# Performance work log

Measured on AMD Instinct MI355X. Metric: run time of the kernel, lower is better.

## Reference

```python
import jax, jax.numpy as jnp
import numpy as np

N_EMBD = 1024
N_HEAD = 16
B, T = 4, 2048

def setup_inputs() -> dict:
    key = jax.random.key(0)
    ks = jax.random.split(key, 5)
    C = N_EMBD
    s = 0.02
    return {
        "x": jax.random.normal(ks[0], (B, T, C), dtype=jnp.float32),
        "W_attn": jax.random.normal(ks[1], (C, 3 * C), dtype=jnp.float32) * s,
        "b_attn": jnp.zeros((3 * C,), dtype=jnp.float32),
        "W_proj": jax.random.normal(ks[2], (C, C), dtype=jnp.float32) * s,
        "b_proj": jnp.zeros((C,), dtype=jnp.float32),
    }

def reference(x, W_attn, b_attn, W_proj, b_proj):
    Bz, Tz, C = x.shape
    H = N_HEAD
    hd = C // H
    qkv = x @ W_attn + b_attn                      # [B,T,3C]
    q, k, v = jnp.split(qkv, 3, axis=-1)
    # [B,H,T,hd]
    q = q.reshape(Bz, Tz, H, hd).transpose(0, 2, 1, 3)
    k = k.reshape(Bz, Tz, H, hd).transpose(0, 2, 1, 3)
    v = v.reshape(Bz, Tz, H, hd).transpose(0, 2, 1, 3)
    att = jnp.einsum('bhqd,bhkd->bhqk', q, k) * (1.0 / np.sqrt(hd))
    causal = jnp.tril(jnp.ones((Tz, Tz), dtype=bool))
    att = jnp.where(causal, att, -jnp.inf)
    att = jax.nn.softmax(att, axis=-1)
    y = jnp.einsum('bhqk,bhkd->bhqd', att, v)      # [B,H,T,hd]
    y = y.transpose(0, 2, 1, 3).reshape(Bz, Tz, C)
    return y @ W_proj + b_proj
```

## Files before the change

### kernel.cpp

```cpp
#include <hip/hip_runtime.h>
#include <hip/hip_bf16.h>

#define NEMBD 1024
#define NHEAD 16
#define HD    64
#define BB    4
#define TT    2048
#define MM    (BB*TT)
#define NQKV  (3*NEMBD)

typedef unsigned short u16;
typedef __attribute__((ext_vector_type(8))) short short8;
typedef __attribute__((ext_vector_type(4))) float floatx4;
typedef __attribute__((ext_vector_type(16))) float floatx16;

__device__ __forceinline__ u16 f2bf(float f) {
    __hip_bfloat16 h = __float2bfloat16(f);
    return *reinterpret_cast<u16*>(&h);
}

__device__ __forceinline__ unsigned pack_bf16(float a, float b) {
    __hip_bfloat162 h2 = __float22bfloat162_rn(float2{a, b});
    return *reinterpret_cast<unsigned*>(&h2);
}

__device__ __forceinline__ unsigned trunc_pack(float a, float b) {
    return __builtin_amdgcn_perm(__float_as_uint(b), __float_as_uint(a), 0x07060302u);
}

__device__ __forceinline__ void gl_lds16(const u16* g, u16* l) {
    __builtin_amdgcn_global_load_lds(
        (const __attribute__((address_space(1))) unsigned int*)g,
        (__attribute__((address_space(3))) unsigned int*)l,
        16, 0, 0);
}

__device__ __forceinline__ short8 scale8(short8 f, float c) {
    union { short8 s; unsigned u[4]; } a, r;
    a.s = f;
    for (int i = 0; i < 4; i++) {
        float lo = __uint_as_float(a.u[i] << 16) * c;
        float hi = __uint_as_float(a.u[i] & 0xffff0000u) * c;
        r.u[i] = pack_bf16(lo, hi);
    }
    return r.s;
}

__global__ __launch_bounds__(256) void cast_f32_bf16(const float* __restrict__ in,
                                                     u16* __restrict__ out, int n) {
    int i = (blockIdx.x * 256 + threadIdx.x) * 4;
    if (i < n) {
        float4 v = *(const float4*)(in + i);
        uint2 o;
        o.x = pack_bf16(v.x, v.y);
        o.y = pack_bf16(v.z, v.w);
        *(uint2*)(out + i) = o;
    }
}

__global__ __launch_bounds__(256) void transpose_cast(const float* __restrict__ in,
                                                      u16* __restrict__ out, int K, int N) {
    __shared__ float tile[32][33];
    int n0 = blockIdx.x * 32, k0 = blockIdx.y * 32;
    int tx = threadIdx.x, ty = threadIdx.y;
    for (int i = 0; i < 4; i++)
        tile[ty + i * 8][tx] = in[(k0 + ty + i * 8) * N + n0 + tx];
    __syncthreads();
    for (int i = 0; i < 4; i++)
        out[(n0 + ty + i * 8) * K + k0 + tx] = f2bf(tile[tx][ty + i * 8]);
}

template <int EPI>
__global__ __launch_bounds__(256)
void gemm_bt(const u16* __restrict__ A, const u16* __restrict__ Bt,
             const float* __restrict__ bias, void* __restrict__ out0,
             u16* __restrict__ outK, u16* __restrict__ outV) {
    const int K = NEMBD;
    __shared__ u16 As[128 * 64];
    __shared__ u16 Bs[128 * 64];
    int tid = threadIdx.x;
    int lane = tid & 63, w = tid >> 6;
    int l32 = lane & 31, lhi = lane >> 5;
    int wm = w >> 1, wn = w & 1;
    int bM = blockIdx.y * 128, bN = blockIdx.x * 128;

    floatx16 acc[2][2];
    for (int i = 0; i < 2; i++)
        for (int j = 0; j < 2; j++)
            acc[i][j] = (floatx16)(0.f);

    int srow = lane >> 3;
    int scol = ((lane & 7) ^ srow) * 8;
    const u16* Ag = A  + (size_t)(bM + w * 32 + srow) * K + scol;
    const u16* Bg = Bt + (size_t)(bN + w * 32 + srow) * K + scol;

    int physo[4];
    for (int kc = 0; kc < 4; kc++)
        physo[kc] = ((kc * 2 + lhi) ^ (lane & 7)) * 8;

    for (int k0 = 0; k0 < K; k0 += 64) {
        for (int i = 0; i < 4; i++) {
            gl_lds16(Ag + (size_t)i * 8 * K + k0, &As[(w * 32 + i * 8) * 64]);
            gl_lds16(Bg + (size_t)i * 8 * K + k0, &Bs[(w * 32 + i * 8) * 64]);
        }
        __syncthreads();
        for (int kc = 0; kc < 4; kc++) {
            short8 af[2], bf[2];
            for (int i = 0; i < 2; i++)
                af[i] = *(const short8*)&As[(wm * 64 + i * 32 + l32) * 64 + physo[kc]];
            for (int j = 0; j < 2; j++)
                bf[j] = *(const short8*)&Bs[(wn * 64 + j * 32 + l32) * 64 + physo[kc]];
            for (int i = 0; i < 2; i++)
                for (int j = 0; j < 2; j++)
                    acc[i][j] = __builtin_amdgcn_mfma_f32_32x32x16_bf16(af[i], bf[j], acc[i][j], 0, 0, 0);
        }
        __syncthreads();
    }

    for (int j = 0; j < 2; j++) {
        int n = bN + wn * 64 + j * 32 + l32;
        float bv = bias[n];
        for (int i = 0; i < 2; i++) {
            int mbase = bM + wm * 64 + i * 32 + 4 * lhi;
            for (int reg = 0; reg < 16; reg++) {
                float v = acc[i][j][reg] + bv;
                int mg = mbase + (reg & 3) + 8 * (reg >> 2);
                if (EPI == 0) {
                    int which = n >> 10, c = n & 1023;
                    int h = c >> 6, d = c & 63;
                    int b = mg >> 11, t = mg & 2047;
                    u16* dst = (which == 0) ? (u16*)out0 : (which == 1 ? outK : outV);
                    dst[(((size_t)(b * NHEAD + h) * TT) + t) * HD + d] = f2bf(v);
                } else {
                    ((float*)out0)[(size_t)mg * NEMBD + n] = v;
                }
            }
        }
    }
}

__global__ __launch_bounds__(256, 2)
void attn_kernel(const u16* __restrict__ Q, const u16* __restrict__ Kg,
                 const u16* __restrict__ V, u16* __restrict__ Y) {
    __shared__ u16 Ks[2][64][72];
    __shared__ u16 Vt[2][64][72];
    __shared__ u16 Ps[4][32][72];

    int tid = threadIdx.x;
    int lane = tid & 63, w = tid >> 6;
    int quad = lane >> 4, l16 = lane & 15;
    int bh = blockIdx.y;
    int ib = blockIdx.x;
    int qa0 = ib * 128;
    int qb0 = (15 - ib) * 128;
    const u16* Qb = Q  + (size_t)bh * TT * HD;
    const u16* Kb = Kg + (size_t)bh * TT * HD;
    const u16* Vb = V  + (size_t)bh * TT * HD;
    int wqa = qa0 + w * 32;
    int wqb = qb0 + w * 32;

    const float C = 0.18033688f;

    short8 qfa[2][2], qfb[2][2];
    for (int qt = 0; qt < 2; qt++)
        for (int kd = 0; kd < 2; kd++) {
            qfa[qt][kd] = scale8(*(const short8*)(Qb + (size_t)(wqa + qt * 16 + l16) * HD + kd * 32 + quad * 8), C);
            qfb[qt][kd] = scale8(*(const short8*)(Qb + (size_t)(wqb + qt * 16 + l16) * HD + kd * 32 + quad * 8), C);
        }

    floatx4 oa[4][2], ob[4][2];
    for (int dt = 0; dt < 4; dt++)
        for (int qt = 0; qt < 2; qt++) {
            oa[dt][qt] = (floatx4){0.f, 0.f, 0.f, 0.f};
            ob[dt][qt] = (floatx4){0.f, 0.f, 0.f, 0.f};
        }
    float la[2] = {0.f, 0.f};
    float lb[2] = {0.f, 0.f};

    int krow = tid >> 2, kcg = (tid & 3) * 16;
    int vkp = (tid & 31) * 2, vd0 = (tid >> 5) * 8;

    auto stage_write = [&](int bp, uint4 k0v, uint4 k1v, uint4 v0, uint4 v1) {
        *(uint4*)&Ks[bp][krow][kcg]     = k0v;
        *(uint4*)&Ks[bp][krow][kcg + 8] = k1v;
        const unsigned* w0p = (const unsigned*)&v0;
        const unsigned* w1p = (const unsigned*)&v1;
        for (int e = 0; e < 4; e++) {
            *(unsigned*)&Vt[bp][vd0 + 2 * e][vkp]     = __builtin_amdgcn_perm(w1p[e], w0p[e], 0x05040100u);
            *(unsigned*)&Vt[bp][vd0 + 2 * e + 1][vkp] = __builtin_amdgcn_perm(w1p[e], w0p[e], 0x07060302u);
        }
    };

    auto process = [&](int k0, int wq0, short8 (&qf)[2][2], short8 (&kf)[4][2],
                       const u16 (*Vtp)[72], floatx4 (&o)[4][2], float (&l_s)[2]) {
        floatx4 s[2][4];
        for (int qt = 0; qt < 2; qt++)
            for (int kt = 0; kt < 4; kt++) {
                floatx4 a = (floatx4){0.f, 0.f, 0.f, 0.f};
                a = __builtin_amdgcn_mfma_f32_16x16x32_bf16(kf[kt][0], qf[qt][0], a, 0, 0, 0);
                a = __builtin_amdgcn_mfma_f32_16x16x32_bf16(kf[kt][1], qf[qt][1], a, 0, 0, 0);
                s[qt][kt] = a;
            }

        bool diag = (k0 + 64 > wq0);
        for (int qt = 0; qt < 2; qt++) {
            int qg = wq0 + qt * 16 + l16;
            if (diag) {
                for (int kt = 0; kt < 4; kt++)
                    for (int r = 0; r < 4; r++)
                        if (k0 + kt * 16 + quad * 4 + r > qg) s[qt][kt][r] = -INFINITY;
            }
            float rs = 0.f;
            for (int kt = 0; kt < 4; kt++)
                for (int r = 0; r < 4; r++) {
                    float p = exp2f(s[qt][kt][r]);
                    s[qt][kt][r] = p;
                    rs += p;
                }
            l_s[qt] += rs;
        }

        for (int qt = 0; qt < 2; qt++)
            for (int kt = 0; kt < 4; kt++) {
                floatx4 p = s[qt][kt];
                *(unsigned*)&Ps[w][qt * 16 + l16][kt * 16 + quad * 4]     = trunc_pack(p[0], p[1]);
                *(unsigned*)&Ps[w][qt * 16 + l16][kt * 16 + quad * 4 + 2] = trunc_pack(p[2], p[3]);
            }
        short8 pfrag[2][2];
        for (int qt = 0; qt < 2; qt++)
            for (int c = 0; c < 2; c++)
                pfrag[qt][c] = *(const short8*)&Ps[w][qt * 16 + l16][c * 32 + quad * 8];
        for (int c = 0; c < 2; c++)
            for (int dt = 0; dt < 4; dt++) {
                short8 vfrag = *(const short8*)&Vtp[dt * 16 + l16][c * 32 + quad * 8];
                for (int qt = 0; qt < 2; qt++)
                    o[dt][qt] = __builtin_amdgcn_mfma_f32_16x16x32_bf16(vfrag, pfrag[qt][c], o[dt][qt], 0, 0, 0);
            }
    };

    {
        uint4 k0v = *(const uint4*)(Kb + (size_t)krow * HD + kcg);
        uint4 k1v = *(const uint4*)(Kb + (size_t)krow * HD + kcg + 8);
        uint4 v0  = *(const uint4*)(Vb + (size_t)vkp * HD + vd0);
        uint4 v1  = *(const uint4*)(Vb + (size_t)(vkp + 1) * HD + vd0);
        stage_write(0, k0v, k1v, v0, v1);
    }
    __syncthreads();

    int kend = qb0 + 128;
    int p = 0;
    for (int k0 = 0; k0 < kend; k0 += 64, p ^= 1) {
        bool pref = (k0 + 64 < kend);
        uint4 nk0, nk1, nv0, nv1;
        if (pref) {
            nk0 = *(const uint4*)(Kb + (size_t)(k0 + 64 + krow) * HD + kcg);
            nk1 = *(const uint4*)(Kb + (size_t)(k0 + 64 + krow) * HD + kcg + 8);
            nv0 = *(const uint4*)(Vb + (size_t)(k0 + 64 + vkp) * HD + vd0);
            nv1 = *(const uint4*)(Vb + (size_t)(k0 + 64 + vkp + 1) * HD + vd0);
        }

        bool acta = (k0 < qa0 + 128) && (k0 < wqa + 32);
        bool actb = (k0 < wqb + 32);
        if (acta || actb) {
            short8 kf[4][2];
            for (int kt = 0; kt < 4; kt++)
                for (int kd = 0; kd < 2; kd++)
                    kf[kt][kd] = *(const short8*)&Ks[p][kt * 16 + l16][kd * 32 + quad * 8];
            if (acta) process(k0, wqa, qfa, kf, Vt[p], oa, la);
            if (actb) process(k0, wqb, qfb, kf, Vt[p], ob, lb);
        }

        if (pref) stage_write(p ^ 1, nk0, nk1, nv0, nv1);
        __syncthreads();
    }

    int b = bh >> 4, h = bh & 15;
    for (int half = 0; half < 2; half++) {
        floatx4 (&o)[4][2] = half ? ob : oa;
        float* l_s = half ? lb : la;
        int wq0 = half ? wqb : wqa;
        for (int qt = 0; qt < 2; qt++) {
            float lt = l_s[qt];
            lt += __shfl_xor(lt, 16, 64);
            lt += __shfl_xor(lt, 32, 64);
            float inv = 1.0f / lt;
            int qg = wq0 + qt * 16 + l16;
            size_t base = ((size_t)(b * TT + qg)) * NEMBD + h * HD;
            for (int dt = 0; dt < 4; dt++) {
                *(unsigned*)&Y[base + dt * 16 + quad * 4]     = pack_bf16(o[dt][qt][0] * inv, o[dt][qt][1] * inv);
                *(unsigned*)&Y[base + dt * 16 + quad * 4 + 2] = pack_bf16(o[dt][qt][2] * inv, o[dt][qt][3] * inv);
            }
        }
    }
}

extern "C" void kernel_launch(void* const* d_in, const int* in_sizes, int n_in,
                              void* d_out, int out_size, void* d_ws, size_t ws_size,
                              hipStream_t stream) {
    const float* x      = (const float*)d_in[0];
    const float* W_attn = (const float*)d_in[1];
    const float* b_attn = (const float*)d_in[2];
    const float* W_proj = (const float*)d_in[3];
    const float* b_proj = (const float*)d_in[4];
    float* out = (float*)d_out;

    char* ws = (char*)d_ws;
    u16* xb  = (u16*)(ws + 0);
    u16* wat = (u16*)(ws + 16777216);
    u16* wpt = (u16*)(ws + 23068672);
    u16* Qb  = (u16*)(ws + 25165824);
    u16* Kb  = (u16*)(ws + 41943040);
    u16* Vb  = (u16*)(ws + 58720256);

    cast_f32_bf16<<<(MM * NEMBD / 4 + 255) / 256, 256, 0, stream>>>(x, xb, MM * NEMBD);
    dim3 tb(32, 8);
    transpose_cast<<<dim3(NQKV / 32, NEMBD / 32), tb, 0, stream>>>(W_attn, wat, NEMBD, NQKV);
    transpose_cast<<<dim3(NEMBD / 32, NEMBD / 32), tb, 0, stream>>>(W_proj, wpt, NEMBD, NEMBD);

    gemm_bt<0><<<dim3(NQKV / 128, MM / 128), 256, 0, stream>>>(xb, wat, b_attn, (void*)Qb, Kb, Vb);
    attn_kernel<<<dim3(8, BB * NHEAD), 256, 0, stream>>>(Qb, Kb, Vb, xb);
    gemm_bt<1><<<dim3(NEMBD / 128, MM / 128), 256, 0, stream>>>(xb, wpt, b_proj, (void*)out, nullptr, nullptr);
}
```

Baseline: 247.5 us.

## Split paired causal query tiles into separate blocks with single-buffered K/V

Drops the pairing of a short and a long causal query tile per block. Each block now handles one 128-row query tile, ordered longest first, and the grid doubles to 16 blocks per head. The K/V shared buffers go from double to single buffering, with an extra barrier between compute and staging. The launch bound is raised to 4 blocks per SM to gain occupancy, at the cost of tighter register limits, less reuse of each K/V tile, and load imbalance between the blocks now being handled by the scheduler.

New measurement: 340.9 us. +37.8%, slower.

```diff
diff --git a/kernel.cpp b/kernel.cpp
--- a/kernel.cpp
+++ b/kernel.cpp
@@ -139,60 +139,57 @@
     }
 }
 
-__global__ __launch_bounds__(256, 2)
+__global__ __launch_bounds__(256, 4)
 void attn_kernel(const u16* __restrict__ Q, const u16* __restrict__ Kg,
                  const u16* __restrict__ V, u16* __restrict__ Y) {
-    __shared__ u16 Ks[2][64][72];
-    __shared__ u16 Vt[2][64][72];
+    __shared__ u16 Ks[64][72];
+    __shared__ u16 Vt[64][72];
     __shared__ u16 Ps[4][32][72];
 
     int tid = threadIdx.x;
     int lane = tid & 63, w = tid >> 6;
     int quad = lane >> 4, l16 = lane & 15;
     int bh = blockIdx.y;
-    int ib = blockIdx.x;
-    int qa0 = ib * 128;
-    int qb0 = (15 - ib) * 128;
+    int jq = 15 - blockIdx.x;
+    int q0 = jq * 128;
     const u16* Qb = Q  + (size_t)bh * TT * HD;
     const u16* Kb = Kg + (size_t)bh * TT * HD;
     const u16* Vb = V  + (size_t)bh * TT * HD;
-    int wqa = qa0 + w * 32;
-    int wqb = qb0 + w * 32;
+    int wq = q0 + w * 32;
 
     const float C = 0.18033688f;
 
-    short8 qfa[2][2], qfb[2][2];
+    short8 qf[2][2];
     for (int qt = 0; qt < 2; qt++)
-        for (int kd = 0; kd < 2; kd++) {
-            qfa[qt][kd] = scale8(*(const short8*)(Qb + (size_t)(wqa + qt * 16 + l16) * HD + kd * 32 + quad * 8), C);
-            qfb[qt][kd] = scale8(*(const short8*)(Qb + (size_t)(wqb + qt * 16 + l16) * HD + kd * 32 + quad * 8), C);
-        }
-
-    floatx4 oa[4][2], ob[4][2];
+        for (int kd = 0; kd < 2; kd++)
+            qf[qt][kd] = scale8(*(const short8*)(Qb + (size_t)(wq + qt * 16 + l16) * HD + kd * 32 + quad * 8), C);
+
+    floatx4 o[4][2];
     for (int dt = 0; dt < 4; dt++)
-        for (int qt = 0; qt < 2; qt++) {
-            oa[dt][qt] = (floatx4){0.f, 0.f, 0.f, 0.f};
-            ob[dt][qt] = (floatx4){0.f, 0.f, 0.f, 0.f};
-        }
-    float la[2] = {0.f, 0.f};
-    float lb[2] = {0.f, 0.f};
+        for (int qt = 0; qt < 2; qt++)
+            o[dt][qt] = (floatx4){0.f, 0.f, 0.f, 0.f};
+    float l_s[2] = {0.f, 0.f};
 
     int krow = tid >> 2, kcg = (tid & 3) * 16;
     int vkp = (tid & 31) * 2, vd0 = (tid >> 5) * 8;
 
-    auto stage_write = [&](int bp, uint4 k0v, uint4 k1v, uint4 v0, uint4 v1) {
-        *(uint4*)&Ks[bp][krow][kcg]     = k0v;
-        *(uint4*)&Ks[bp][krow][kcg + 8] = k1v;
+    auto stage_write = [&](uint4 k0v, uint4 k1v, uint4 v0, uint4 v1) {
+        *(uint4*)&Ks[krow][kcg]     = k0v;
+        *(uint4*)&Ks[krow][kcg + 8] = k1v;
         const unsigned* w0p = (const unsigned*)&v0;
         const unsigned* w1p = (const unsigned*)&v1;
         for (int e = 0; e < 4; e++) {
-            *(unsigned*)&Vt[bp][vd0 + 2 * e][vkp]     = __builtin_amdgcn_perm(w1p[e], w0p[e], 0x05040100u);
-            *(unsigned*)&Vt[bp][vd0 + 2 * e + 1][vkp] = __builtin_amdgcn_perm(w1p[e], w0p[e], 0x07060302u);
+            *(unsigned*)&Vt[vd0 + 2 * e][vkp]     = __builtin_amdgcn_perm(w1p[e], w0p[e], 0x05040100u);
+            *(unsigned*)&Vt[vd0 + 2 * e + 1][vkp] = __builtin_amdgcn_perm(w1p[e], w0p[e], 0x07060302u);
         }
     };
 
-    auto process = [&](int k0, int wq0, short8 (&qf)[2][2], short8 (&kf)[4][2],
-                       const u16 (*Vtp)[72], floatx4 (&o)[4][2], float (&l_s)[2]) {
+    auto process = [&](int k0) {
+        short8 kf[4][2];
+        for (int kt = 0; kt < 4; kt++)
+            for (int kd = 0; kd < 2; kd++)
+                kf[kt][kd] = *(const short8*)&Ks[kt * 16 + l16][kd * 32 + quad * 8];
+
         floatx4 s[2][4];
         for (int qt = 0; qt < 2; qt++)
             for (int kt = 0; kt < 4; kt++) {
@@ -202,9 +199,9 @@
                 s[qt][kt] = a;
             }
 
-        bool diag = (k0 + 64 > wq0);
+        bool diag = (k0 + 64 > wq);
         for (int qt = 0; qt < 2; qt++) {
-            int qg = wq0 + qt * 16 + l16;
+            int qg = wq + qt * 16 + l16;
             if (diag) {
                 for (int kt = 0; kt < 4; kt++)
                     for (int r = 0; r < 4; r++)
@@ -232,7 +229,7 @@
                 pfrag[qt][c] = *(const short8*)&Ps[w][qt * 16 + l16][c * 32 + quad * 8];
         for (int c = 0; c < 2; c++)
             for (int dt = 0; dt < 4; dt++) {
-                short8 vfrag = *(const short8*)&Vtp[dt * 16 + l16][c * 32 + quad * 8];
+                short8 vfrag = *(const short8*)&Vt[dt * 16 + l16][c * 32 + quad * 8];
                 for (int qt = 0; qt < 2; qt++)
                     o[dt][qt] = __builtin_amdgcn_mfma_f32_16x16x32_bf16(vfrag, pfrag[qt][c], o[dt][qt], 0, 0, 0);
             }
@@ -243,13 +240,12 @@
         uint4 k1v = *(const uint4*)(Kb + (size_t)krow * HD + kcg + 8);
         uint4 v0  = *(const uint4*)(Vb + (size_t)vkp * HD + vd0);
         uint4 v1  = *(const uint4*)(Vb + (size_t)(vkp + 1) * HD + vd0);
-        stage_write(0, k0v, k1v, v0, v1);
+        stage_write(k0v, k1v, v0, v1);
     }
     __syncthreads();
 
-    int kend = qb0 + 128;
-    int p = 0;
-    for (int k0 = 0; k0 < kend; k0 += 64, p ^= 1) {
+    int kend = q0 + 128;
+    for (int k0 = 0; k0 < kend; k0 += 64) {
         bool pref = (k0 + 64 < kend);
         uint4 nk0, nk1, nv0, nv1;
         if (pref) {
@@ -259,37 +255,26 @@
             nv1 = *(const uint4*)(Vb + (size_t)(k0 + 64 + vkp + 1) * HD + vd0);
         }
 
-        bool acta = (k0 < qa0 + 128) && (k0 < wqa + 32);
-        bool actb = (k0 < wqb + 32);
-        if (acta || actb) {
-            short8 kf[4][2];
-            for (int kt = 0; kt < 4; kt++)
-                for (int kd = 0; kd < 2; kd++)
-                    kf[kt][kd] = *(const short8*)&Ks[p][kt * 16 + l16][kd * 32 + quad * 8];
-            if (acta) process(k0, wqa, qfa, kf, Vt[p], oa, la);
-            if (actb) process(k0, wqb, qfb, kf, Vt[p], ob, lb);
-        }
-
-        if (pref) stage_write(p ^ 1, nk0, nk1, nv0, nv1);
+        if (k0 < wq + 32) process(k0);
+
         __syncthreads();
+        if (pref) {
+            stage_write(nk0, nk1, nv0, nv1);
+        }
+        __syncthreads();
     }
 
     int b = bh >> 4, h = bh & 15;
-    for (int half = 0; half < 2; half++) {
-        floatx4 (&o)[4][2] = half ? ob : oa;
-        float* l_s = half ? lb : la;
-        int wq0 = half ? wqb : wqa;
-        for (int qt = 0; qt < 2; qt++) {
-            float lt = l_s[qt];
-            lt += __shfl_xor(lt, 16, 64);
-            lt += __shfl_xor(lt, 32, 64);
-            float inv = 1.0f / lt;
-            int qg = wq0 + qt * 16 + l16;
-            size_t base = ((size_t)(b * TT + qg)) * NEMBD + h * HD;
-            for (int dt = 0; dt < 4; dt++) {
-                *(unsigned*)&Y[base + dt * 16 + quad * 4]     = pack_bf16(o[dt][qt][0] * inv, o[dt][qt][1] * inv);
-                *(unsigned*)&Y[base + dt * 16 + quad * 4 + 2] = pack_bf16(o[dt][qt][2] * inv, o[dt][qt][3] * inv);
-            }
+    for (int qt = 0; qt < 2; qt++) {
+        float lt = l_s[qt];
+        lt += __shfl_xor(lt, 16, 64);
+        lt += __shfl_xor(lt, 32, 64);
+        float inv = 1.0f / lt;
+        int qg = wq + qt * 16 + l16;
+        size_t base = ((size_t)(b * TT + qg)) * NEMBD + h * HD;
+        for (int dt = 0; dt < 4; dt++) {
+            *(unsigned*)&Y[base + dt * 16 + quad * 4]     = pack_bf16(o[dt][qt][0] * inv, o[dt][qt][1] * inv);
+            *(unsigned*)&Y[base + dt * 16 + quad * 4 + 2] = pack_bf16(o[dt][qt][2] * inv, o[dt][qt][3] * inv);
         }
     }
 }
@@ -318,6 +303,6 @@
     transpose_cast<<<dim3(NEMBD / 32, NEMBD / 32), tb, 0, stream>>>(W_proj, wpt, NEMBD, NEMBD);
 
     gemm_bt<0><<<dim3(NQKV / 128, MM / 128), 256, 0, stream>>>(xb, wat, b_attn, (void*)Qb, Kb, Vb);
-    attn_kernel<<<dim3(8, BB * NHEAD), 256, 0, stream>>>(Qb, Kb, Vb, xb);
+    attn_kernel<<<dim3(16, BB * NHEAD), 256, 0, stream>>>(Qb, Kb, Vb, xb);
     gemm_bt<1><<<dim3(NEMBD / 128, MM / 128), 256, 0, stream>>>(xb, wpt, b_proj, (void*)out, nullptr, nullptr);
 }
```
